# Kernel optimization log

Hardware: AMD Instinct MI355X
Metric: run time of the kernel (lower is better)

## Reference

```python
import jax, jax.numpy as jnp
import numpy as np

B, N, Q, D, H = 8, 2048, 256, 1024, 16
HD = D // H


def setup_inputs() -> dict:
    key = jax.random.key(0)
    ks = jax.random.split(key, 6)
    scale = 1.0 / np.sqrt(D)
    return {
        "sources": jax.random.normal(ks[0], (B, N, D), dtype=jnp.float32),
        "queries": jax.random.normal(ks[1], (B, Q, D), dtype=jnp.float32),
        "w_in": jax.random.normal(ks[2], (3 * D, D), dtype=jnp.float32) * scale,
        "b_in": jax.random.normal(ks[3], (3 * D,), dtype=jnp.float32) * 0.02,
        "w_out": jax.random.normal(ks[4], (D, D), dtype=jnp.float32) * scale,
        "b_out": jax.random.normal(ks[5], (D,), dtype=jnp.float32) * 0.02,
    }


def reference(sources, queries, w_in, b_in, w_out, b_out):
    # torch nn.MultiheadAttention (batch_first, eval mode, no attn_mask),
    # applied per-sample with equal lengths == one batched cross-attention.
    w_q, w_k, w_v = jnp.split(w_in, 3, axis=0)   # each [D, D]
    b_q, b_k, b_v = jnp.split(b_in, 3, axis=0)
    q = queries @ w_q.T + b_q                    # [B, Q, D]
    k = sources @ w_k.T + b_k                    # [B, N, D]
    v = sources @ w_v.T + b_v                    # [B, N, D]
    q = q.reshape(B, Q, H, HD)
    k = k.reshape(B, N, H, HD)
    v = v.reshape(B, N, H, HD)
    scale = 1.0 / np.sqrt(HD).astype(np.float32)
    scores = jnp.einsum("bqhd,bkhd->bhqk", q, k) * scale  # [B, H, Q, N]
    attn = jax.nn.softmax(scores, axis=-1)
    out = jnp.einsum("bhqk,bkhd->bqhd", attn, v).reshape(B, Q, D)
    out = out @ w_out.T + b_out                  # out_proj
    return out + queries                         # residual (fix=False: no norm)
```

## Files before the change

kernel.cpp:

```cpp
#include <hip/hip_runtime.h>
#include <hip/hip_bf16.h>


typedef unsigned short u16;
typedef __attribute__((ext_vector_type(8))) short short8;
typedef __attribute__((ext_vector_type(4))) float floatx4;

static_assert(sizeof(short8) == 16, "short8 must be 16B");

__device__ __forceinline__ u16 f2bf(float f) {
  unsigned int x = __float_as_uint(f);
  x += 0x7fffu + ((x >> 16) & 1u);
  return (u16)(x >> 16);
}

__device__ __forceinline__ unsigned int cvtpk(float lo, float hi) {
  unsigned int r;
  asm("v_cvt_pk_bf16_f32 %0, %1, %2" : "=v"(r) : "v"(lo), "v"(hi));
  return r;
}

__device__ __forceinline__ void gload16(const u16* g, u16* lds) {
  __builtin_amdgcn_global_load_lds(
      (const __attribute__((address_space(1))) unsigned int*)g,
      (__attribute__((address_space(3))) unsigned int*)lds, 16, 0, 0);
}

template <int N> __device__ __forceinline__ void vmwait() {
  if constexpr (N == 0)      asm volatile("s_waitcnt vmcnt(0)" ::: "memory");
  else if constexpr (N == 2) asm volatile("s_waitcnt vmcnt(2)" ::: "memory");
  else if constexpr (N == 4) asm volatile("s_waitcnt vmcnt(4)" ::: "memory");
  else if constexpr (N == 6) asm volatile("s_waitcnt vmcnt(6)" ::: "memory");
  else if constexpr (N == 8) asm volatile("s_waitcnt vmcnt(8)" ::: "memory");
  else static_assert(N == 0, "unsupported vmcnt immediate");
}

__device__ __forceinline__ void lgkm0() {
  asm volatile("s_waitcnt lgkmcnt(0)" ::: "memory");
}

__device__ __forceinline__ void sfence() { __builtin_amdgcn_sched_barrier(0); }

__global__ __launch_bounds__(256) void f2bf_multi(
    const float* __restrict__ s, u16* __restrict__ so,
    const float* __restrict__ q, u16* __restrict__ qo,
    const float* __restrict__ wi, u16* __restrict__ wio,
    const float* __restrict__ wo, u16* __restrict__ woo) {
  int i = blockIdx.x * 256 + threadIdx.x;
  const float* in; u16* out; int idx;
  if (i < 4194304)      { in = s;  out = so;  idx = i; }
  else if (i < 4718592) { in = q;  out = qo;  idx = i - 4194304; }
  else if (i < 5505024) { in = wi; out = wio; idx = i - 4718592; }
  else if (i < 5767168) { in = wo; out = woo; idx = i - 5505024; }
  else return;
  float4 v = reinterpret_cast<const float4*>(in)[idx];
  ushort4 o;
  o.x = f2bf(v.x); o.y = f2bf(v.y); o.z = f2bf(v.z); o.w = f2bf(v.w);
  reinterpret_cast<ushort4*>(out)[idx] = o;
}

template <int MT, int NT>
__device__ __forceinline__ void gemm_core(
    const u16* __restrict__ A, int lda,
    const u16* __restrict__ Bm, int ldb, int K,
    u16* __restrict__ Alds, u16* __restrict__ Blds,
    floatx4 (&acc)[MT][NT]) {
  const int t = threadIdx.x;
  const int wave = t >> 6, lane = t & 63;
  const int rr = lane & 15, kq = lane >> 4;
  constexpr int AI = MT, BI = NT;
  constexpr int AELEMS = MT * 32 * 64;
  constexpr int BELEMS = NT * 32 * 64;

  const u16* ag[AI]; u16* al[AI];
#pragma unroll
  for (int i = 0; i < AI; ++i) {
    int s = i * 256 + t;
    int row = s >> 3, c16 = s & 7;
    ag[i] = A + (size_t)row * lda + ((c16 ^ (row & 7)) * 8);
    al[i] = Alds + (size_t)(i * 256 + wave * 64) * 8;
  }
  const u16* bg[BI]; u16* blp[BI];
#pragma unroll
  for (int i = 0; i < BI; ++i) {
    int s = i * 256 + t;
    int row = s >> 3, c16 = s & 7;
    bg[i] = Bm + (size_t)row * ldb + ((c16 ^ (row & 7)) * 8);
    blp[i] = Blds + (size_t)(i * 256 + wave * 64) * 8;
  }

  const int m0w = (wave & 1) * (MT * 16);
  const int n0w = (wave >> 1) * (NT * 16);
  int aoff[MT][2], boff[NT][2];
#pragma unroll
  for (int mi = 0; mi < MT; ++mi) {
    int row = m0w + mi * 16 + rr;
#pragma unroll
    for (int kk = 0; kk < 2; ++kk)
      aoff[mi][kk] = row * 64 + (((kk * 4 + kq) ^ (row & 7)) * 8);
  }
#pragma unroll
  for (int ni = 0; ni < NT; ++ni) {
    int row = n0w + ni * 16 + rr;
#pragma unroll
    for (int kk = 0; kk < 2; ++kk)
      boff[ni][kk] = row * 64 + (((kk * 4 + kq) ^ (row & 7)) * 8);
  }

  auto compute = [&](int bs) {
    const u16* Ab = Alds + bs * AELEMS;
    const u16* Bb = Blds + bs * BELEMS;
#pragma unroll
    for (int kk = 0; kk < 2; ++kk) {
      short8 af[MT], bfr[NT];
#pragma unroll
      for (int mi = 0; mi < MT; ++mi)
        af[mi] = *reinterpret_cast<const short8*>(Ab + aoff[mi][kk]);
#pragma unroll
      for (int ni = 0; ni < NT; ++ni)
        bfr[ni] = *reinterpret_cast<const short8*>(Bb + boff[ni][kk]);
      __builtin_amdgcn_s_setprio(1);
#pragma unroll
      for (int mi = 0; mi < MT; ++mi)
#pragma unroll
        for (int ni = 0; ni < NT; ++ni)
          acc[mi][ni] = __builtin_amdgcn_mfma_f32_16x16x32_bf16(af[mi], bfr[ni], acc[mi][ni], 0, 0, 0);
      __builtin_amdgcn_s_setprio(0);
    }
  };

  const int nt = K >> 6;

#pragma unroll
  for (int i = 0; i < AI; ++i) gload16(ag[i], al[i]);
#pragma unroll
  for (int i = 0; i < BI; ++i) gload16(bg[i], blp[i]);

  int cur = 0;
#pragma unroll 1
  for (int tt = 0; tt < nt - 1; ++tt) {
    const int nxt = cur ^ 1;
    const int koff = (tt + 1) * 64;
#pragma unroll
    for (int i = 0; i < AI; ++i) gload16(ag[i] + koff, al[i] + nxt * AELEMS);
#pragma unroll
    for (int i = 0; i < BI; ++i) gload16(bg[i] + koff, blp[i] + nxt * BELEMS);
    sfence();
    vmwait<AI + BI>();
    __builtin_amdgcn_s_barrier();
    sfence();
    compute(cur);
    sfence();
    __builtin_amdgcn_s_barrier();
    cur = nxt;
  }
  sfence();
  vmwait<0>();
  __builtin_amdgcn_s_barrier();
  sfence();
  compute(cur);
}

template <int LO>
__device__ __forceinline__ void read_a8(const u16* ab, int kcol0, int kcol1,
                                        short8 (&af)[8][2]) {
#pragma unroll
  for (int mi = 0; mi < 4; ++mi) {
    af[LO + mi][0] = *reinterpret_cast<const short8*>(ab + (LO + mi) * 1024 + kcol0);
    af[LO + mi][1] = *reinterpret_cast<const short8*>(ab + (LO + mi) * 1024 + kcol1);
  }
}

template <int LO>
__device__ __forceinline__ void read_b8(const u16* bb, int kcol0, int kcol1,
                                        short8 (&bf)[4][2]) {
#pragma unroll
  for (int ni = 0; ni < 2; ++ni) {
    bf[LO + ni][0] = *reinterpret_cast<const short8*>(bb + (LO + ni) * 1024 + kcol0);
    bf[LO + ni][1] = *reinterpret_cast<const short8*>(bb + (LO + ni) * 1024 + kcol1);
  }
}

template <int M0, int N0>
__device__ __forceinline__ void quad8(const short8 (&af)[8][2], const short8 (&bf)[4][2],
                                      floatx4 (&acc)[8][4]) {
  __builtin_amdgcn_s_setprio(1);
#pragma unroll
  for (int kk = 0; kk < 2; ++kk)
#pragma unroll
    for (int mi = 0; mi < 4; ++mi)
#pragma unroll
      for (int ni = 0; ni < 2; ++ni)
        acc[M0 + mi][N0 + ni] = __builtin_amdgcn_mfma_f32_16x16x32_bf16(
            af[M0 + mi][kk], bf[N0 + ni][kk], acc[M0 + mi][N0 + ni], 0, 0, 0);
  __builtin_amdgcn_s_setprio(0);
}

__global__ __launch_bounds__(512, 2) void gemm_proj_kv8(
    const u16* __restrict__ s_bf, const u16* __restrict__ wi_bf,
    const float* __restrict__ b_in,
    u16* __restrict__ kp, u16* __restrict__ vT) {
  __shared__ __attribute__((aligned(16))) u16 Alds[2 * 256 * 64];
  __shared__ __attribute__((aligned(16))) u16 Blds[2 * 256 * 64];

  int bid = blockIdx.y * 8 + blockIdx.x;
  int nb = (bid & 7) * 64 + (bid >> 3);
  const int by = nb >> 3, bx = nb & 7;
  const int mB = by * 256;
  const int nB = bx * 256;
  const u16* Ag = s_bf + (size_t)mB * 1024;
  const u16* Wg = wi_bf + (size_t)(1024 + nB) * 1024;
  const float* bias = b_in + 1024 + nB;

  const int t = threadIdx.x;
  const int w = t >> 6, lane = t & 63;
  const int rr = lane & 15, kq = lane >> 4;
  const int wr = w >> 2, wc = w & 3;

  const u16* ga[2][2]; const u16* gb[2][2];
#pragma unroll
  for (int h = 0; h < 2; ++h)
#pragma unroll
    for (int i = 0; i < 2; ++i) {
      int s = i * 512 + t;
      int row = h * 128 + (s >> 3), c16 = s & 7;
      ga[h][i] = Ag + (size_t)row * 1024 + ((c16 ^ (row & 7)) * 8);
      gb[h][i] = Wg + (size_t)row * 1024 + ((c16 ^ (row & 7)) * 8);
    }

#define STAGE_A8(j, h) { const int d_ = ((j) & 1) * 16384;                         \
    gload16(ga[h][0] + (size_t)(j) * 64, Alds + d_ + (h) * 8192 + w * 512);        \
    gload16(ga[h][1] + (size_t)(j) * 64, Alds + d_ + (h) * 8192 + 4096 + w * 512); }
#define STAGE_B8(j, h) { const int d_ = ((j) & 1) * 16384;                         \
    gload16(gb[h][0] + (size_t)(j) * 64, Blds + d_ + (h) * 8192 + w * 512);        \
    gload16(gb[h][1] + (size_t)(j) * 64, Blds + d_ + (h) * 8192 + 4096 + w * 512); }

  const int kcol0 = ((kq) ^ (rr & 7)) * 8;
  const int kcol1 = ((4 + kq) ^ (rr & 7)) * 8;
  const u16* abase = Alds + (wr * 128 + rr) * 64;
  const u16* bbase = Blds + (wc * 64 + rr) * 64;

  short8 af[8][2], bf[4][2];
  const floatx4 zz = {0.f, 0.f, 0.f, 0.f};
  floatx4 acc[8][4];
#pragma unroll
  for (int mi = 0; mi < 8; ++mi)
#pragma unroll
    for (int ni = 0; ni < 4; ++ni) acc[mi][ni] = zz;

  STAGE_A8(0, 0); STAGE_B8(0, 0); STAGE_A8(0, 1); STAGE_B8(0, 1);
  STAGE_A8(1, 0); STAGE_B8(1, 0);
  sfence();
  vmwait<4>();
  __builtin_amdgcn_s_barrier();
  sfence();

#pragma unroll 1
  for (int kt = 0; kt < 16; ++kt) {
    const int doff = (kt & 1) * 16384;
    const u16* ab = abase + doff;
    const u16* bb = bbase + doff;
    read_a8<0>(ab, kcol0, kcol1, af);
    read_b8<0>(bb, kcol0, kcol1, bf);
    if (kt + 1 < 16) STAGE_A8(kt + 1, 1);
    sfence();
    __builtin_amdgcn_s_barrier();
    lgkm0(); sfence();
    quad8<0, 0>(af, bf, acc);
    sfence();
    __builtin_amdgcn_s_barrier();
    sfence();
    read_a8<4>(ab, kcol0, kcol1, af);
    read_b8<2>(bb, kcol0, kcol1, bf);
    if (kt + 1 < 16) STAGE_B8(kt + 1, 1);
    sfence();
    __builtin_amdgcn_s_barrier();
    lgkm0(); sfence();
    quad8<0, 2>(af, bf, acc);
    sfence();
    __builtin_amdgcn_s_barrier();
    sfence();
    if (kt + 2 < 16) STAGE_A8(kt + 2, 0);
    sfence();
    __builtin_amdgcn_s_barrier();
    quad8<4, 0>(af, bf, acc);
    sfence();
    __builtin_amdgcn_s_barrier();
    sfence();
    if (kt + 2 < 16) { STAGE_B8(kt + 2, 0); sfence(); vmwait<4>(); }
    else             { sfence(); vmwait<0>(); }
    __builtin_amdgcn_s_barrier();
    quad8<4, 2>(af, bf, acc);
    sfence();
    __builtin_amdgcn_s_barrier();
    sfence();
  }
#undef STAGE_A8
#undef STAGE_B8

  const int r4 = kq * 4;
  const int m0w = wr * 128, n0w = wc * 64;
  if (nB < 1024) {
#pragma unroll
    for (int mi = 0; mi < 8; ++mi)
#pragma unroll
      for (int ni = 0; ni < 4; ++ni) {
        int nl = n0w + ni * 16 + rr;
        float bv = bias[nl];
#pragma unroll
        for (int r = 0; r < 4; ++r) {
          int m = mB + m0w + mi * 16 + r4 + r;
          kp[(size_t)m * 1024 + nB + nl] = f2bf(acc[mi][ni][r] + bv);
        }
      }
  } else {
#pragma unroll
    for (int mi = 0; mi < 8; ++mi)
#pragma unroll
      for (int ni = 0; ni < 4; ++ni) {
        int n2 = nB + n0w + ni * 16 + rr - 1024;
        int h = n2 >> 6, d = n2 & 63;
        float bv = bias[n0w + ni * 16 + rr];
        int m0 = mB + m0w + mi * 16 + r4;
        int b = m0 >> 11, j0 = m0 & 2047;
        ushort4 o;
        o.x = f2bf(acc[mi][ni][0] + bv);
        o.y = f2bf(acc[mi][ni][1] + bv);
        o.z = f2bf(acc[mi][ni][2] + bv);
        o.w = f2bf(acc[mi][ni][3] + bv);
        *reinterpret_cast<ushort4*>(
            vT + ((size_t)(b * 16 + h) * 64 + d) * 2048 + j0) = o;
      }
  }
}

__global__ __launch_bounds__(256, 2) void gemm_proj_q(
    const u16* __restrict__ qy_bf, const u16* __restrict__ wi_bf,
    const float* __restrict__ b_in, u16* __restrict__ qp) {
  __shared__ __attribute__((aligned(16))) u16 Alds[2 * 128 * 64];
  __shared__ __attribute__((aligned(16))) u16 Blds[2 * 128 * 64];
  const int mB = blockIdx.y * 128;
  const int nB = blockIdx.x * 128;
  const u16* A = qy_bf + (size_t)mB * 1024;
  const u16* W = wi_bf + (size_t)nB * 1024;
  const float* bias = b_in + nB;

  const floatx4 zz = {0.f, 0.f, 0.f, 0.f};
  floatx4 acc[4][4] = {{zz, zz, zz, zz}, {zz, zz, zz, zz}, {zz, zz, zz, zz}, {zz, zz, zz, zz}};
  gemm_core<4, 4>(A, 1024, W, 1024, 1024, Alds, Blds, acc);

  const int lane = threadIdx.x & 63, wave = threadIdx.x >> 6;
  const int rr = lane & 15, r4 = (lane >> 4) * 4;
  const int m0w = (wave & 1) * 64, n0w = (wave >> 1) * 64;
#pragma unroll
  for (int mi = 0; mi < 4; ++mi)
#pragma unroll
    for (int ni = 0; ni < 4; ++ni) {
      int nl = n0w + ni * 16 + rr;
      float bv = bias[nl];
#pragma unroll
      for (int r = 0; r < 4; ++r) {
        int m = mB + m0w + mi * 16 + r4 + r;
        qp[(size_t)m * 1024 + nB + nl] = f2bf((acc[mi][ni][r] + bv) * 0.125f);
      }
    }
}

__global__ __launch_bounds__(512, 4) void attn_fused(
    const u16* __restrict__ qp, const u16* __restrict__ kp,
    const u16* __restrict__ vT, u16* __restrict__ ao) {
  __shared__ __attribute__((aligned(16))) u16 Plds[8192];

  const int bid = blockIdx.x;
  const int nb = (bid & 7) * 64 + (bid >> 3);
  const int bh = nb >> 2, qb = nb & 3;
  const int b = bh >> 4, h = bh & 15;

  const int t = threadIdx.x;
  const int w = t >> 6, lane = t & 63;
  const int rr = lane & 15, kq = lane >> 4;
  const int wk = w >> 1, wq = w & 1;
  const int wPq = w >> 2, wPd = w & 3;

  const u16* qbase = qp + ((size_t)(b * 256 + qb * 64)) * 1024 + h * 64;
  const u16* kbase = kp + ((size_t)b * 2048) * 1024 + h * 64;
  const u16* vbase = vT + ((size_t)bh * 64) * 2048;

  const u16* qg;
  { int row = t >> 3, c8 = t & 7;
    qg = qbase + (size_t)row * 1024 + ((c8 ^ (row & 7)) * 8); }

  const u16* kfp = kbase + (size_t)(wk * 32 + rr) * 1024 + kq * 8;
  const u16* vfp = vbase + (size_t)(wPd * 16 + rr) * 2048 + kq * 8;

  gload16(qg, Plds + w * 512);
  short8 kf[2][2], vf[4];
#pragma unroll
  for (int mi = 0; mi < 2; ++mi)
#pragma unroll
    for (int kc = 0; kc < 2; ++kc)
      kf[mi][kc] = *reinterpret_cast<const short8*>(kfp + (size_t)mi * 16384 + kc * 32);
#pragma unroll
  for (int kc = 0; kc < 4; ++kc)
    vf[kc] = *reinterpret_cast<const short8*>(vfp + kc * 32);
  sfence();
  vmwait<8>();
  __builtin_amdgcn_s_barrier();
  sfence();
  short8 qf[2][2];
#pragma unroll
  for (int ni = 0; ni < 2; ++ni) {
    int qrow = wq * 32 + ni * 16 + rr;
#pragma unroll
    for (int kc = 0; kc < 2; ++kc)
      qf[ni][kc] = *reinterpret_cast<const short8*>(
          Plds + qrow * 64 + (((kc * 4 + kq) ^ (qrow & 7)) * 8));
  }
  lgkm0(); sfence();
  __builtin_amdgcn_s_barrier();
  sfence();

  const short ov = (rr == 0) ? (short)0x3F80 : (short)0;
  const short8 ones = {ov, ov, ov, ov, ov, ov, ov, ov};
  const floatx4 zz = {0.f, 0.f, 0.f, 0.f};
  floatx4 oacc[2] = {zz, zz};
  floatx4 acc_l[2] = {zz, zz};

  const int pq0 = wq * 32 + rr;
  const int pkb = wk * 4 + (kq >> 1);
  const int pk4 = (kq & 1) * 4;

#pragma unroll 1
  for (int kt = 0; kt < 16; ++kt) {
    floatx4 sacc[2][2] = {{zz, zz}, {zz, zz}};
    __builtin_amdgcn_s_setprio(1);
#pragma unroll
    for (int kc = 0; kc < 2; ++kc)
#pragma unroll
      for (int mi = 0; mi < 2; ++mi)
#pragma unroll
        for (int ni = 0; ni < 2; ++ni)
          sacc[mi][ni] = __builtin_amdgcn_mfma_f32_16x16x32_bf16(
              kf[mi][kc], qf[ni][kc], sacc[mi][ni], 0, 0, 0);
    __builtin_amdgcn_s_setprio(0);
    if (kt + 1 < 16) {
      const u16* kp2 = kfp + (size_t)(kt + 1) * 131072;
#pragma unroll
      for (int mi = 0; mi < 2; ++mi)
#pragma unroll
        for (int kc = 0; kc < 2; ++kc)
          kf[mi][kc] = *reinterpret_cast<const short8*>(kp2 + (size_t)mi * 16384 + kc * 32);
    }
    sfence();
#pragma unroll
    for (int mi = 0; mi < 2; ++mi) {
      int kb = pkb + mi * 2;
#pragma unroll
      for (int ni = 0; ni < 2; ++ni) {
        int q = pq0 + ni * 16;
        float e0 = __expf(sacc[mi][ni][0]);
        float e1 = __expf(sacc[mi][ni][1]);
        float e2 = __expf(sacc[mi][ni][2]);
        float e3 = __expf(sacc[mi][ni][3]);
        uint2 pv;
        pv.x = cvtpk(e0, e1);
        pv.y = cvtpk(e2, e3);
        *reinterpret_cast<uint2*>(
            &Plds[q * 128 + ((kb ^ (q & 7)) << 3) + pk4]) = pv;
      }
    }
    lgkm0(); sfence();
    __builtin_amdgcn_s_barrier();
    sfence();
    short8 pa[2][4];
#pragma unroll
    for (int mi = 0; mi < 2; ++mi) {
      int qrow = wPq * 32 + mi * 16 + rr;
#pragma unroll
      for (int kc = 0; kc < 4; ++kc)
        pa[mi][kc] = *reinterpret_cast<const short8*>(
            Plds + qrow * 128 + (((kc * 4 + kq) ^ (qrow & 7)) << 3));
    }
    __builtin_amdgcn_s_setprio(1);
#pragma unroll
    for (int kc = 0; kc < 4; ++kc)
#pragma unroll
      for (int mi = 0; mi < 2; ++mi) {
        oacc[mi] = __builtin_amdgcn_mfma_f32_16x16x32_bf16(
            pa[mi][kc], vf[kc], oacc[mi], 0, 0, 0);
        acc_l[mi] = __builtin_amdgcn_mfma_f32_16x16x32_bf16(
            pa[mi][kc], ones, acc_l[mi], 0, 0, 0);
      }
    __builtin_amdgcn_s_setprio(0);
    if (kt + 1 < 16) {
      const u16* vp2 = vfp + (size_t)(kt + 1) * 128;
#pragma unroll
      for (int kc = 0; kc < 4; ++kc)
        vf[kc] = *reinterpret_cast<const short8*>(vp2 + kc * 32);
    }
    sfence();
    __builtin_amdgcn_s_barrier();
    sfence();
  }

  u16* aob = ao + ((size_t)(b * 256 + qb * 64)) * 1024 + h * 64;
#pragma unroll
  for (int mi = 0; mi < 2; ++mi)
#pragma unroll
    for (int r = 0; r < 4; ++r) {
      float l = __shfl(acc_l[mi][r], lane & 48, 64);
      float inv = 1.0f / l;
      int q = wPq * 32 + mi * 16 + kq * 4 + r;
      int d = wPd * 16 + rr;
      aob[(size_t)q * 1024 + d] = f2bf(oacc[mi][r] * inv);
    }
}

__global__ __launch_bounds__(256, 2) void gemm_out(
    const u16* __restrict__ A, const u16* __restrict__ W,
    const float* __restrict__ bias, const float* __restrict__ resid,
    float* __restrict__ out) {
  __shared__ __attribute__((aligned(16))) u16 Alds[2 * 64 * 64];
  __shared__ __attribute__((aligned(16))) u16 Blds[2 * 128 * 64];
  const int mB = blockIdx.y * 64;
  const int nB = blockIdx.x * 128;
  const floatx4 zz = {0.f, 0.f, 0.f, 0.f};
  floatx4 acc[2][4] = {{zz, zz, zz, zz}, {zz, zz, zz, zz}};
  gemm_core<2, 4>(A + (size_t)mB * 1024, 1024, W + (size_t)nB * 1024, 1024, 1024,
                  Alds, Blds, acc);
  const int lane = threadIdx.x & 63, wave = threadIdx.x >> 6;
  const int rr = lane & 15, r4 = (lane >> 4) * 4;
  const int m0w = (wave & 1) * 32, n0w = (wave >> 1) * 64;
#pragma unroll
  for (int mi = 0; mi < 2; ++mi)
#pragma unroll
    for (int ni = 0; ni < 4; ++ni) {
      int n = nB + n0w + ni * 16 + rr;
      float bv = bias[n];
#pragma unroll
      for (int r = 0; r < 4; ++r) {
        int m = mB + m0w + mi * 16 + r4 + r;
        size_t idx = (size_t)m * 1024 + n;
        out[idx] = acc[mi][ni][r] + bv + resid[idx];
      }
    }
}

extern "C" void kernel_launch(void* const* d_in, const int* in_sizes, int n_in,
                              void* d_out, int out_size, void* d_ws, size_t ws_size,
                              hipStream_t stream) {
  const float* sources = (const float*)d_in[0];
  const float* queries = (const float*)d_in[1];
  const float* w_in    = (const float*)d_in[2];
  const float* b_in    = (const float*)d_in[3];
  const float* w_out   = (const float*)d_in[4];
  const float* b_out   = (const float*)d_in[5];
  float* out = (float*)d_out;

  char* ws = (char*)d_ws;
  size_t off = 0;
  auto alloc = [&](size_t elems) -> u16* {
    u16* p = (u16*)(ws + off);
    off += elems * sizeof(u16);
    off = (off + 255) & ~(size_t)255;
    return p;
  };
  u16* s_bf  = alloc((size_t)16777216);
  u16* qy_bf = alloc((size_t)2097152);
  u16* wi_bf = alloc((size_t)3145728);
  u16* wo_bf = alloc((size_t)1048576);
  u16* qp    = alloc((size_t)2097152);
  u16* kp    = alloc((size_t)16777216);
  u16* vT    = alloc((size_t)16777216);
  u16* ao    = alloc((size_t)2097152);

  f2bf_multi<<<dim3(22528), 256, 0, stream>>>(
      sources, s_bf, queries, qy_bf, w_in, wi_bf, w_out, wo_bf);

  gemm_proj_kv8<<<dim3(8, 64), 512, 0, stream>>>(s_bf, wi_bf, b_in, kp, vT);
  gemm_proj_q<<<dim3(8, 16), 256, 0, stream>>>(qy_bf, wi_bf, b_in, qp);

  attn_fused<<<dim3(512), 512, 0, stream>>>(qp, kp, vT, ao);

  gemm_out<<<dim3(8, 32), 256, 0, stream>>>(ao, wo_bf, b_out, queries, out);
}
```

Before: 296.1 us.

## Rewrite attention kernel as per-wave register-resident loop without LDS or barriers

The attention kernel is restructured so each of four waves owns 16 query rows and walks all 2048 keys in 32-key steps. K and V are loaded directly from global memory every iteration, and P is moved from the score layout to the operand layout with cross-lane shuffles instead of an LDS round trip. This removes the shared-memory buffer, all block barriers and the MFMA against a ones vector, computing the row sum with scalar adds instead. In exchange there is no K/V prefetch or register double-buffering, so each iteration waits on global load latency. Each wave also re-reads K/V that was previously shared across waves, raising cache traffic.

```diff
diff --git a/kernel.cpp b/kernel.cpp
--- a/kernel.cpp
+++ b/kernel.cpp
@@ -5,6 +5,7 @@
 typedef unsigned short u16;
 typedef __attribute__((ext_vector_type(8))) short short8;
 typedef __attribute__((ext_vector_type(4))) float floatx4;
+typedef __attribute__((ext_vector_type(4))) int intx4;
 
 static_assert(sizeof(short8) == 16, "short8 must be 16B");
 
@@ -28,7 +29,6 @@
 
 template <int N> __device__ __forceinline__ void vmwait() {
   if constexpr (N == 0)      asm volatile("s_waitcnt vmcnt(0)" ::: "memory");
-  else if constexpr (N == 2) asm volatile("s_waitcnt vmcnt(2)" ::: "memory");
   else if constexpr (N == 4) asm volatile("s_waitcnt vmcnt(4)" ::: "memory");
   else if constexpr (N == 6) asm volatile("s_waitcnt vmcnt(6)" ::: "memory");
   else if constexpr (N == 8) asm volatile("s_waitcnt vmcnt(8)" ::: "memory");
@@ -366,154 +366,100 @@
     }
 }
 
-__global__ __launch_bounds__(512, 4) void attn_fused(
+__global__ __launch_bounds__(256, 4) void attn_fused(
     const u16* __restrict__ qp, const u16* __restrict__ kp,
     const u16* __restrict__ vT, u16* __restrict__ ao) {
-  __shared__ __attribute__((aligned(16))) u16 Plds[8192];
-
   const int bid = blockIdx.x;
   const int nb = (bid & 7) * 64 + (bid >> 3);
-  const int bh = nb >> 2, qb = nb & 3;
+  const int bh = nb >> 2, qq = nb & 3;
   const int b = bh >> 4, h = bh & 15;
 
   const int t = threadIdx.x;
   const int w = t >> 6, lane = t & 63;
   const int rr = lane & 15, kq = lane >> 4;
-  const int wk = w >> 1, wq = w & 1;
-  const int wPq = w >> 2, wPd = w & 3;
-
-  const u16* qbase = qp + ((size_t)(b * 256 + qb * 64)) * 1024 + h * 64;
-  const u16* kbase = kp + ((size_t)b * 2048) * 1024 + h * 64;
-  const u16* vbase = vT + ((size_t)bh * 64) * 2048;
-
-  const u16* qg;
-  { int row = t >> 3, c8 = t & 7;
-    qg = qbase + (size_t)row * 1024 + ((c8 ^ (row & 7)) * 8); }
-
-  const u16* kfp = kbase + (size_t)(wk * 32 + rr) * 1024 + kq * 8;
-  const u16* vfp = vbase + (size_t)(wPd * 16 + rr) * 2048 + kq * 8;
-
-  gload16(qg, Plds + w * 512);
-  short8 kf[2][2], vf[4];
-#pragma unroll
-  for (int mi = 0; mi < 2; ++mi)
-#pragma unroll
-    for (int kc = 0; kc < 2; ++kc)
-      kf[mi][kc] = *reinterpret_cast<const short8*>(kfp + (size_t)mi * 16384 + kc * 32);
-#pragma unroll
-  for (int kc = 0; kc < 4; ++kc)
-    vf[kc] = *reinterpret_cast<const short8*>(vfp + kc * 32);
-  sfence();
-  vmwait<8>();
-  __builtin_amdgcn_s_barrier();
-  sfence();
-  short8 qf[2][2];
-#pragma unroll
-  for (int ni = 0; ni < 2; ++ni) {
-    int qrow = wq * 32 + ni * 16 + rr;
-#pragma unroll
-    for (int kc = 0; kc < 2; ++kc)
-      qf[ni][kc] = *reinterpret_cast<const short8*>(
-          Plds + qrow * 64 + (((kc * 4 + kq) ^ (qrow & 7)) * 8));
-  }
-  lgkm0(); sfence();
-  __builtin_amdgcn_s_barrier();
-  sfence();
-
-  const short ov = (rr == 0) ? (short)0x3F80 : (short)0;
-  const short8 ones = {ov, ov, ov, ov, ov, ov, ov, ov};
+  const int q0 = qq * 64 + w * 16;
+
+  const u16* qrow = qp + ((size_t)(b * 256 + q0 + rr)) * 1024 + h * 64 + kq * 8;
+  short8 qf[2];
+  qf[0] = *reinterpret_cast<const short8*>(qrow);
+  qf[1] = *reinterpret_cast<const short8*>(qrow + 32);
+
+  const u16* kbase = kp + ((size_t)(b * 2048 + rr)) * 1024 + h * 64 + kq * 8;
+  const u16* vbase = vT + ((size_t)(bh * 64 + rr)) * 2048 + kq * 8;
+
   const floatx4 zz = {0.f, 0.f, 0.f, 0.f};
-  floatx4 oacc[2] = {zz, zz};
-  floatx4 acc_l[2] = {zz, zz};
-
-  const int pq0 = wq * 32 + rr;
-  const int pkb = wk * 4 + (kq >> 1);
-  const int pk4 = (kq & 1) * 4;
+  floatx4 oacc[4] = {zz, zz, zz, zz};
+  float l_acc = 0.f;
+
+  const int sel = kq >> 1;
+  const int sb = rr + ((kq & 1) << 5);
 
 #pragma unroll 1
-  for (int kt = 0; kt < 16; ++kt) {
-    floatx4 sacc[2][2] = {{zz, zz}, {zz, zz}};
-    __builtin_amdgcn_s_setprio(1);
-#pragma unroll
-    for (int kc = 0; kc < 2; ++kc)
-#pragma unroll
-      for (int mi = 0; mi < 2; ++mi)
-#pragma unroll
-        for (int ni = 0; ni < 2; ++ni)
-          sacc[mi][ni] = __builtin_amdgcn_mfma_f32_16x16x32_bf16(
-              kf[mi][kc], qf[ni][kc], sacc[mi][ni], 0, 0, 0);
-    __builtin_amdgcn_s_setprio(0);
-    if (kt + 1 < 16) {
-      const u16* kp2 = kfp + (size_t)(kt + 1) * 131072;
-#pragma unroll
-      for (int mi = 0; mi < 2; ++mi)
-#pragma unroll
-        for (int kc = 0; kc < 2; ++kc)
-          kf[mi][kc] = *reinterpret_cast<const short8*>(kp2 + (size_t)mi * 16384 + kc * 32);
+  for (int kt = 0; kt < 64; ++kt) {
+    const u16* kp0 = kbase + (size_t)(kt * 32) * 1024;
+    short8 kf0 = *reinterpret_cast<const short8*>(kp0);
+    short8 kf1 = *reinterpret_cast<const short8*>(kp0 + 32);
+    short8 kf2 = *reinterpret_cast<const short8*>(kp0 + 16 * 1024);
+    short8 kf3 = *reinterpret_cast<const short8*>(kp0 + 16 * 1024 + 32);
+    const u16* vp0 = vbase + kt * 32;
+    short8 vf0 = *reinterpret_cast<const short8*>(vp0);
+    short8 vf1 = *reinterpret_cast<const short8*>(vp0 + 16 * 2048);
+    short8 vf2 = *reinterpret_cast<const short8*>(vp0 + 32 * 2048);
+    short8 vf3 = *reinterpret_cast<const short8*>(vp0 + 48 * 2048);
+
+    floatx4 sacc0 = zz, sacc1 = zz;
+    sacc0 = __builtin_amdgcn_mfma_f32_16x16x32_bf16(kf0, qf[0], sacc0, 0, 0, 0);
+    sacc0 = __builtin_amdgcn_mfma_f32_16x16x32_bf16(kf1, qf[1], sacc0, 0, 0, 0);
+    sacc1 = __builtin_amdgcn_mfma_f32_16x16x32_bf16(kf2, qf[0], sacc1, 0, 0, 0);
+    sacc1 = __builtin_amdgcn_mfma_f32_16x16x32_bf16(kf3, qf[1], sacc1, 0, 0, 0);
+
+    unsigned u00 = cvtpk(__expf(sacc0[0]), __expf(sacc0[1]));
+    unsigned u01 = cvtpk(__expf(sacc0[2]), __expf(sacc0[3]));
+    unsigned u10 = cvtpk(__expf(sacc1[0]), __expf(sacc1[1]));
+    unsigned u11 = cvtpk(__expf(sacc1[2]), __expf(sacc1[3]));
+
+    l_acc += __uint_as_float(u00 << 16) + __uint_as_float(u00 & 0xffff0000u)
+           + __uint_as_float(u01 << 16) + __uint_as_float(u01 & 0xffff0000u)
+           + __uint_as_float(u10 << 16) + __uint_as_float(u10 & 0xffff0000u)
+           + __uint_as_float(u11 << 16) + __uint_as_float(u11 & 0xffff0000u);
+
+    unsigned a0 = (unsigned)__shfl((int)u00, sb);
+    unsigned b0 = (unsigned)__shfl((int)u10, sb);
+    unsigned a1 = (unsigned)__shfl((int)u01, sb);
+    unsigned b1 = (unsigned)__shfl((int)u11, sb);
+    unsigned a2 = (unsigned)__shfl((int)u00, sb + 16);
+    unsigned b2 = (unsigned)__shfl((int)u10, sb + 16);
+    unsigned a3 = (unsigned)__shfl((int)u01, sb + 16);
+    unsigned b3 = (unsigned)__shfl((int)u11, sb + 16);
+    intx4 pw;
+    pw.x = (int)(sel ? b0 : a0);
+    pw.y = (int)(sel ? b1 : a1);
+    pw.z = (int)(sel ? b2 : a2);
+    pw.w = (int)(sel ? b3 : a3);
+    union { intx4 i; short8 s; } pa;
+    pa.i = pw;
+
+    oacc[0] = __builtin_amdgcn_mfma_f32_16x16x32_bf16(pa.s, vf0, oacc[0], 0, 0, 0);
+    oacc[1] = __builtin_amdgcn_mfma_f32_16x16x32_bf16(pa.s, vf1, oacc[1], 0, 0, 0);
+    oacc[2] = __builtin_amdgcn_mfma_f32_16x16x32_bf16(pa.s, vf2, oacc[2], 0, 0, 0);
+    oacc[3] = __builtin_amdgcn_mfma_f32_16x16x32_bf16(pa.s, vf3, oacc[3], 0, 0, 0);
+  }
+
+  l_acc += __shfl_xor(l_acc, 16);
+  l_acc += __shfl_xor(l_acc, 32);
+
+  u16* aob = ao + ((size_t)(b * 256 + q0)) * 1024 + h * 64;
+#pragma unroll
+  for (int r = 0; r < 4; ++r) {
+    float lv = __shfl(l_acc, kq * 4 + r);
+    float inv = 1.0f / lv;
+    int qrow_o = kq * 4 + r;
+#pragma unroll
+    for (int ni = 0; ni < 4; ++ni) {
+      int d = ni * 16 + rr;
+      aob[(size_t)qrow_o * 1024 + d] = f2bf(oacc[ni][r] * inv);
     }
-    sfence();
-#pragma unroll
-    for (int mi = 0; mi < 2; ++mi) {
-      int kb = pkb + mi * 2;
-#pragma unroll
-      for (int ni = 0; ni < 2; ++ni) {
-        int q = pq0 + ni * 16;
-        float e0 = __expf(sacc[mi][ni][0]);
-        float e1 = __expf(sacc[mi][ni][1]);
-        float e2 = __expf(sacc[mi][ni][2]);
-        float e3 = __expf(sacc[mi][ni][3]);
-        uint2 pv;
-        pv.x = cvtpk(e0, e1);
-        pv.y = cvtpk(e2, e3);
-        *reinterpret_cast<uint2*>(
-            &Plds[q * 128 + ((kb ^ (q & 7)) << 3) + pk4]) = pv;
-      }
-    }
-    lgkm0(); sfence();
-    __builtin_amdgcn_s_barrier();
-    sfence();
-    short8 pa[2][4];
-#pragma unroll
-    for (int mi = 0; mi < 2; ++mi) {
-      int qrow = wPq * 32 + mi * 16 + rr;
-#pragma unroll
-      for (int kc = 0; kc < 4; ++kc)
-        pa[mi][kc] = *reinterpret_cast<const short8*>(
-            Plds + qrow * 128 + (((kc * 4 + kq) ^ (qrow & 7)) << 3));
-    }
-    __builtin_amdgcn_s_setprio(1);
-#pragma unroll
-    for (int kc = 0; kc < 4; ++kc)
-#pragma unroll
-      for (int mi = 0; mi < 2; ++mi) {
-        oacc[mi] = __builtin_amdgcn_mfma_f32_16x16x32_bf16(
-            pa[mi][kc], vf[kc], oacc[mi], 0, 0, 0);
-        acc_l[mi] = __builtin_amdgcn_mfma_f32_16x16x32_bf16(
-            pa[mi][kc], ones, acc_l[mi], 0, 0, 0);
-      }
-    __builtin_amdgcn_s_setprio(0);
-    if (kt + 1 < 16) {
-      const u16* vp2 = vfp + (size_t)(kt + 1) * 128;
-#pragma unroll
-      for (int kc = 0; kc < 4; ++kc)
-        vf[kc] = *reinterpret_cast<const short8*>(vp2 + kc * 32);
-    }
-    sfence();
-    __builtin_amdgcn_s_barrier();
-    sfence();
-  }
-
-  u16* aob = ao + ((size_t)(b * 256 + qb * 64)) * 1024 + h * 64;
-#pragma unroll
-  for (int mi = 0; mi < 2; ++mi)
-#pragma unroll
-    for (int r = 0; r < 4; ++r) {
-      float l = __shfl(acc_l[mi][r], lane & 48, 64);
-      float inv = 1.0f / l;
-      int q = wPq * 32 + mi * 16 + kq * 4 + r;
-      int d = wPd * 16 + rr;
-      aob[(size_t)q * 1024 + d] = f2bf(oacc[mi][r] * inv);
-    }
+  }
 }
 
 __global__ __launch_bounds__(256, 2) void gemm_out(
@@ -580,7 +526,7 @@
   gemm_proj_kv8<<<dim3(8, 64), 512, 0, stream>>>(s_bf, wi_bf, b_in, kp, vT);
   gemm_proj_q<<<dim3(8, 16), 256, 0, stream>>>(qy_bf, wi_bf, b_in, qp);
 
-  attn_fused<<<dim3(512), 512, 0, stream>>>(qp, kp, vT, ao);
+  attn_fused<<<dim3(512), 256, 0, stream>>>(qp, kp, vT, ao);
 
   gemm_out<<<dim3(8, 32), 256, 0, stream>>>(ao, wo_bf, b_out, queries, out);
 }
```

Measured after the change: 347.6 us. 1.17x slower.
